# Optimization experiments

Hardware: AMD Instinct MI355X
Metric: run time of the kernel (lower is better)

The kernel has to match this reference:

```python
import jax, jax.numpy as jnp
import numpy as np

B, N, DIM, HEADS, DEPTH, MLP = 4, 1024, 256, 4, 4, 1024
DH = DIM // HEADS
EPS = 1e-5


def _ln(x, g, b):
    mu = jnp.mean(x, axis=-1, keepdims=True)
    var = jnp.mean((x - mu) ** 2, axis=-1, keepdims=True)
    return (x - mu) / jnp.sqrt(var + EPS) * g + b


def setup_inputs() -> dict:
    key = jax.random.key(0)
    ks = jax.random.split(key, 10)
    s = 0.02
    p = {}
    p["x"] = jax.random.normal(ks[0], (B, N, DIM), jnp.float32)
    p["attn_bias"] = jax.random.normal(ks[1], (2, B, HEADS, N, N), jnp.float32)
    p["ln1_g"] = jnp.ones((DEPTH, DIM), jnp.float32)
    p["ln1_b"] = jnp.zeros((DEPTH, DIM), jnp.float32)
    p["Wkv"] = jax.random.normal(ks[2], (DEPTH, DIM, 2 * DIM), jnp.float32) * s
    p["Wq"] = jax.random.normal(ks[3], (DEPTH, DIM, DIM), jnp.float32) * s
    p["Wo"] = jax.random.normal(ks[4], (DEPTH, DIM, DIM), jnp.float32) * s
    p["bo"] = jnp.zeros((DEPTH, DIM), jnp.float32)
    p["ln2_g"] = jnp.ones((DEPTH, DIM), jnp.float32)
    p["ln2_b"] = jnp.zeros((DEPTH, DIM), jnp.float32)
    p["W1"] = jax.random.normal(ks[5], (DEPTH, DIM, MLP), jnp.float32) * s
    p["b1"] = jnp.zeros((DEPTH, MLP), jnp.float32)
    p["W2"] = jax.random.normal(ks[6], (DEPTH, MLP, DIM), jnp.float32) * s
    p["b2"] = jnp.zeros((DEPTH, DIM), jnp.float32)
    p["Wg"] = jax.random.normal(ks[7], (DIM, DIM), jnp.float32) * s
    p["lng_g"] = jnp.ones((DIM,), jnp.float32)
    p["lng_b"] = jnp.zeros((DIM,), jnp.float32)
    return p


def reference(x, attn_bias, ln1_g, ln1_b, Wkv, Wq, Wo, bo, ln2_g, ln2_b, W1, b1, W2, b2, Wg, lng_g, lng_b):
    scale = DIM ** -0.5
    add_attn = attn_bias[0] + attn_bias[1]            # [B,H,N,N]
    # aggregation bias matrices are layer-invariant (recomputed identically each layer in torch)
    A = jnp.mean(attn_bias[0], axis=1)                # [B,N,N]
    S = jnp.mean(attn_bias[1], axis=1)
    G = jax.nn.softmax(A * S, axis=2)                 # [B,N,N]

    def split_heads(t):  # [B,N,DIM] -> [B,H,N,DH]
        return t.reshape(B, N, HEADS, DH).transpose(0, 2, 1, 3)

    for l in range(DEPTH):
        # softmax-GCN aggregation
        x_ma = jax.nn.relu(_ln(jnp.matmul(G, x) @ Wg, lng_g, lng_b))
        # attention (PreNorm on x only; q comes from un-normed x_ma)
        xn = _ln(x, ln1_g[l], ln1_b[l])
        kv = xn @ Wkv[l]
        k, v = jnp.split(kv, 2, axis=-1)
        q = x_ma @ Wq[l]
        qh, kh, vh = split_heads(q), split_heads(k), split_heads(v)
        dots = jnp.einsum('bhid,bhjd->bhij', qh, kh) * scale + add_attn
        attn = jax.nn.softmax(dots, axis=-1)
        out = jnp.einsum('bhij,bhjd->bhid', attn, vh)
        out = out.transpose(0, 2, 1, 3).reshape(B, N, DIM)
        x = x + out @ Wo[l] + bo[l]
        # feed-forward (exact GELU, matching torch nn.GELU default)
        xn2 = _ln(x, ln2_g[l], ln2_b[l])
        x = x + jax.nn.gelu(xn2 @ W1[l] + b1[l], approximate=False) @ W2[l] + b2[l]
    return x
```

## Files before the change

### kernel.cpp

```cpp
#include <hip/hip_runtime.h>
#include <hip/hip_bf16.h>
#include <math.h>

typedef unsigned short u16;
typedef __bf16 bf16x8 __attribute__((ext_vector_type(8)));
typedef float f32x4 __attribute__((ext_vector_type(4)));

#define B_ 4
#define N_ 1024
#define DIM_ 256
#define HEADS_ 4
#define DH_ 64
#define MLP_ 1024
#define DEPTH_ 4

__device__ __forceinline__ float r2f(u16 r){ return __uint_as_float(((unsigned)r)<<16); }
__device__ __forceinline__ u16 f2r(float f){ __hip_bfloat16 h = __float2bfloat16(f); return *(u16*)&h; }
__device__ __forceinline__ float ldv(const float* p){ return *p; }
__device__ __forceinline__ float ldv(const u16* p){ return r2f(*p); }
__device__ __forceinline__ void stv(float* p, float v){ *p = v; }
__device__ __forceinline__ void stv(u16* p, float v){ *p = f2r(v); }

__device__ __forceinline__ float gelu_exact(float v){
  return 0.5f*v*(1.0f + erff(v*0.70710678118654752440f));
}

#define MFMA16(a,b,c) __builtin_amdgcn_mfma_f32_16x16x32_bf16(a,b,c,0,0,0)

__global__ void copy_f32(const float* __restrict__ in, float* __restrict__ out, int n){
  int i = blockIdx.x*blockDim.x + threadIdx.x;
  if (i < n) out[i] = in[i];
}

__global__ void prep_bias(const float* __restrict__ bias, u16* __restrict__ G, u16* __restrict__ bsum){
  int blk = blockIdx.x;
  int i = blk & (N_-1);
  int b = blk >> 10;
  int t = threadIdx.x;
  __shared__ float sc[N_];
  __shared__ float red[256];
  long long base0 = ((long long)(b*HEADS_)*N_ + i)*(long long)N_;
  const long long hs = (long long)N_*N_;
  const long long cs = (long long)B_*HEADS_*N_*N_;
  float lmax = -3e38f;
  for (int jj=0;jj<4;jj++){
    int j = t + jj*256;
    float a = 0.f, s = 0.f;
    #pragma unroll
    for (int h=0;h<HEADS_;h++){
      float x0 = bias[base0 + h*hs + j];
      float x1 = bias[cs + base0 + h*hs + j];
      a += x0; s += x1;
      bsum[base0 + h*hs + j] = f2r(x0 + x1);
    }
    float v = (a*0.25f)*(s*0.25f);
    sc[j] = v;
    lmax = fmaxf(lmax, v);
  }
  red[t]=lmax; __syncthreads();
  for (int s=128;s>0;s>>=1){ if(t<s) red[t]=fmaxf(red[t],red[t+s]); __syncthreads(); }
  float m = red[0]; __syncthreads();
  float lsum = 0.f;
  for (int jj=0;jj<4;jj++){
    int j = t + jj*256;
    float e = __expf(sc[j]-m);
    sc[j]=e; lsum+=e;
  }
  red[t]=lsum; __syncthreads();
  for (int s=128;s>0;s>>=1){ if(t<s) red[t]+=red[t+s]; __syncthreads(); }
  float inv = 1.0f/red[0];
  u16* Grow = G + ((long long)b*N_ + i)*(long long)N_;
  for (int jj=0;jj<4;jj++){ int j=t+jj*256; Grow[j]=f2r(sc[j]*inv); }
}

template<typename TIN>
__global__ void ln_kernel(const TIN* __restrict__ X, u16* __restrict__ Y,
                          const float* __restrict__ g, const float* __restrict__ bvec, int relu){
  int row = blockIdx.x, t = threadIdx.x;
  __shared__ float red[256];
  float v = ldv(X + (long long)row*DIM_ + t);
  red[t]=v; __syncthreads();
  for (int s=128;s>0;s>>=1){ if(t<s) red[t]+=red[t+s]; __syncthreads(); }
  float mu = red[0]*(1.0f/DIM_); __syncthreads();
  float d = v - mu;
  red[t]=d*d; __syncthreads();
  for (int s=128;s>0;s>>=1){ if(t<s) red[t]+=red[t+s]; __syncthreads(); }
  float var = red[0]*(1.0f/DIM_);
  float y = d*rsqrtf(var+1e-5f)*g[t] + bvec[t];
  if (relu) y = fmaxf(y, 0.0f);
  Y[(long long)row*DIM_ + t] = f2r(y);
}

__global__ void ln_dual(const float* __restrict__ X1, const u16* __restrict__ X2,
                        u16* __restrict__ Y1, u16* __restrict__ Y2,
                        const float* __restrict__ g1, const float* __restrict__ b1v,
                        const float* __restrict__ g2, const float* __restrict__ b2v){
  int blk = blockIdx.x, t = threadIdx.x;
  bool second = blk >= B_*N_;
  int row = second ? blk - B_*N_ : blk;
  __shared__ float red[256];
  float v = second ? r2f(X2[(long long)row*DIM_ + t]) : X1[(long long)row*DIM_ + t];
  red[t]=v; __syncthreads();
  for (int s=128;s>0;s>>=1){ if(t<s) red[t]+=red[t+s]; __syncthreads(); }
  float mu = red[0]*(1.0f/DIM_); __syncthreads();
  float d = v - mu;
  red[t]=d*d; __syncthreads();
  for (int s=128;s>0;s>>=1){ if(t<s) red[t]+=red[t+s]; __syncthreads(); }
  float var = red[0]*(1.0f/DIM_);
  float y;
  if (second){ y = fmaxf(d*rsqrtf(var+1e-5f)*g2[t] + b2v[t], 0.0f); Y2[(long long)row*DIM_+t]=f2r(y); }
  else       { y = d*rsqrtf(var+1e-5f)*g1[t] + b1v[t];              Y1[(long long)row*DIM_+t]=f2r(y); }
}

template<typename TIN>
__global__ void tcast(const TIN* __restrict__ in, u16* __restrict__ out,
                      int ldin, int R, long long sIn, long long sOut){
  __shared__ float tile[32][33];
  int z = blockIdx.z;
  const TIN* I = in + (long long)z*sIn;
  u16* O = out + (long long)z*sOut;
  int c0 = blockIdx.x*32, r0 = blockIdx.y*32;
  int tx = threadIdx.x, ty = threadIdx.y;
  #pragma unroll
  for (int i=0;i<4;i++)
    tile[ty*4+i][tx] = ldv(I + (long long)(r0+ty*4+i)*ldin + c0+tx);
  __syncthreads();
  #pragma unroll
  for (int i=0;i<4;i++)
    O[(long long)(c0+ty*4+i)*R + r0+tx] = f2r(tile[tx][ty*4+i]);
}

template<typename OT, int ACT>
__global__ __launch_bounds__(256) void wgemm(
    const u16* __restrict__ A, const u16* __restrict__ BT, OT* __restrict__ Cb,
    int K, int lda, int ldbt, int ldc, int ZS,
    long long sAb, long long sAh, long long sBb, long long sBh,
    long long sCb, long long sCh,
    const float* __restrict__ colBias, const float* __restrict__ res)
{
  int z = blockIdx.z, zb = z>>ZS, zh = z & ((1<<ZS)-1);
  A  += zb*sAb + zh*sAh;
  BT += zb*sBb + zh*sBh;
  long long co = zb*sCb + zh*sCh;
  int tid = threadIdx.x, w = tid>>6, lane = tid&63;
  int lr = lane&15, qd = lane>>4;
  int m0 = blockIdx.y*64 + (w>>1)*32;
  int n0 = blockIdx.x*64 + (w&1)*32;
  const u16* Ap0 = A  + (long long)(m0+lr)*lda;
  const u16* Ap1 = A  + (long long)(m0+16+lr)*lda;
  const u16* Bp0 = BT + (long long)(n0+lr)*ldbt;
  const u16* Bp1 = BT + (long long)(n0+16+lr)*ldbt;
  f32x4 acc[2][2] = {};
  for (int k0=0; k0<K; k0+=64){
    #pragma unroll
    for (int ks=0; ks<2; ks++){
      int ko = k0 + ks*32 + qd*8;
      bf16x8 a0 = *(const bf16x8*)(Ap0+ko);
      bf16x8 a1 = *(const bf16x8*)(Ap1+ko);
      bf16x8 b0 = *(const bf16x8*)(Bp0+ko);
      bf16x8 b1 = *(const bf16x8*)(Bp1+ko);
      acc[0][0] = MFMA16(a0,b0,acc[0][0]);
      acc[0][1] = MFMA16(a0,b1,acc[0][1]);
      acc[1][0] = MFMA16(a1,b0,acc[1][0]);
      acc[1][1] = MFMA16(a1,b1,acc[1][1]);
    }
  }
  OT* C = Cb + co;
  const float* rs = res ? res + co : nullptr;
  #pragma unroll
  for (int rt=0;rt<2;rt++){
    #pragma unroll
    for (int ct=0;ct<2;ct++){
      int gc = n0 + ct*16 + lr;
      float cb = colBias ? colBias[gc] : 0.f;
      #pragma unroll
      for (int r=0;r<4;r++){
        int gr = m0 + rt*16 + qd*4 + r;
        float v = acc[rt][ct][r] + cb;
        if (ACT) v = gelu_exact(v);
        if (rs) v += rs[(long long)gr*ldc + gc];
        stv(C + (long long)gr*ldc + gc, v);
      }
    }
  }
}

static inline void gemm(hipStream_t st, const u16* A, const u16* BT, void* C, int outBf, int act,
    int M, int N, int K, int lda, int ldbt, int ldc, int Z, int ZS,
    long long sAb, long long sAh, long long sBb, long long sBh, long long sCb, long long sCh,
    const float* cb, const float* res)
{
  dim3 g(N/64, M/64, Z), b(256);
  if (outBf){
    if (act) wgemm<u16,1><<<g,b,0,st>>>(A,BT,(u16*)C,K,lda,ldbt,ldc,ZS,sAb,sAh,sBb,sBh,sCb,sCh,cb,res);
    else     wgemm<u16,0><<<g,b,0,st>>>(A,BT,(u16*)C,K,lda,ldbt,ldc,ZS,sAb,sAh,sBb,sBh,sCb,sCh,cb,res);
  } else {
    if (act) wgemm<float,1><<<g,b,0,st>>>(A,BT,(float*)C,K,lda,ldbt,ldc,ZS,sAb,sAh,sBb,sBh,sCb,sCh,cb,res);
    else     wgemm<float,0><<<g,b,0,st>>>(A,BT,(float*)C,K,lda,ldbt,ldc,ZS,sAb,sAh,sBb,sBh,sCb,sCh,cb,res);
  }
}

__global__ __launch_bounds__(256) void flash_attn(
    const u16* __restrict__ qb, const u16* __restrict__ kvb,
    const u16* __restrict__ vt, const u16* __restrict__ bsum,
    u16* __restrict__ out)
{
  int z = blockIdx.z;
  int b = z>>2, h = z&3;
  int qt = blockIdx.x;
  int tid = threadIdx.x;
  int w = tid>>6, lane = tid&63;
  int lr = lane&15, qd = lane>>4;
  __shared__ u16 Pl[4][16][72];

  int qrow0 = qt*64 + w*16;
  const u16* qp = qb + ((long long)(b*N_) + qrow0 + lr)*DIM_ + h*DH_;
  bf16x8 aq0 = *(const bf16x8*)(qp + qd*8);
  bf16x8 aq1 = *(const bf16x8*)(qp + 32 + qd*8);

  f32x4 oacc[4] = {};
  float m_r[4] = {-3e38f,-3e38f,-3e38f,-3e38f};
  float l_r[4] = {0.f,0.f,0.f,0.f};

  const u16* kbase = kvb + ((long long)(b*N_))*512 + h*DH_;
  const u16* vbase = vt + (long long)b*(DIM_*N_) + (long long)(h*DH_)*N_;
  const u16* bias_base = bsum + ((long long)z*N_ + qrow0)*(long long)N_;

  for (int jt=0; jt<16; jt++){
    int j0 = jt*64;
    f32x4 sacc[4] = {};
    #pragma unroll
    for (int nt=0; nt<4; nt++){
      const u16* kp = kbase + (long long)(j0 + nt*16 + lr)*512;
      bf16x8 bk0 = *(const bf16x8*)(kp + qd*8);
      bf16x8 bk1 = *(const bf16x8*)(kp + 32 + qd*8);
      sacc[nt] = MFMA16(aq0, bk0, sacc[nt]);
      sacc[nt] = MFMA16(aq1, bk1, sacc[nt]);
    }
    #pragma unroll
    for (int r=0;r<4;r++){
      float pv[4];
      float vmax = -3e38f;
      #pragma unroll
      for (int nt=0;nt<4;nt++){
        float v = sacc[nt][r]*0.0625f
                + r2f(bias_base[(long long)(qd*4+r)*N_ + j0 + nt*16 + lr]);
        pv[nt] = v;
        vmax = fmaxf(vmax, v);
      }
      vmax = fmaxf(vmax, __shfl_xor(vmax,1));
      vmax = fmaxf(vmax, __shfl_xor(vmax,2));
      vmax = fmaxf(vmax, __shfl_xor(vmax,4));
      vmax = fmaxf(vmax, __shfl_xor(vmax,8));
      float newm = fmaxf(m_r[r], vmax);
      float alpha = __expf(m_r[r]-newm);
      m_r[r] = newm;
      float psum = 0.f;
      #pragma unroll
      for (int nt=0;nt<4;nt++){
        float p = __expf(pv[nt]-newm);
        psum += p;
        Pl[w][qd*4+r][nt*16+lr] = f2r(p);
      }
      psum += __shfl_xor(psum,1);
      psum += __shfl_xor(psum,2);
      psum += __shfl_xor(psum,4);
      psum += __shfl_xor(psum,8);
      l_r[r] = l_r[r]*alpha + psum;
      #pragma unroll
      for (int ot=0;ot<4;ot++) oacc[ot][r] *= alpha;
    }
    #pragma unroll
    for (int ks=0;ks<2;ks++){
      bf16x8 ap = *(const bf16x8*)&Pl[w][lr][ks*32 + qd*8];
      #pragma unroll
      for (int ot=0;ot<4;ot++){
        const u16* vp = vbase + (long long)(ot*16+lr)*N_ + j0 + ks*32 + qd*8;
        bf16x8 bv = *(const bf16x8*)vp;
        oacc[ot] = MFMA16(ap, bv, oacc[ot]);
      }
    }
  }
  #pragma unroll
  for (int r=0;r<4;r++){
    float inv = 1.0f/l_r[r];
    #pragma unroll
    for (int ot=0;ot<4;ot++){
      out[((long long)(b*N_) + qrow0 + qd*4 + r)*DIM_ + h*DH_ + ot*16 + lr]
          = f2r(oacc[ot][r]*inv);
    }
  }
}

extern "C" void kernel_launch(void* const* d_in, const int* in_sizes, int n_in,
                              void* d_out, int out_size, void* d_ws, size_t ws_size,
                              hipStream_t stream){
  const float* x_in   = (const float*)d_in[0];
  const float* abias  = (const float*)d_in[1];
  const float* ln1_g  = (const float*)d_in[2];
  const float* ln1_b  = (const float*)d_in[3];
  const float* Wkv    = (const float*)d_in[4];
  const float* Wq     = (const float*)d_in[5];
  const float* Wo     = (const float*)d_in[6];
  const float* bo     = (const float*)d_in[7];
  const float* ln2_g  = (const float*)d_in[8];
  const float* ln2_b  = (const float*)d_in[9];
  const float* W1     = (const float*)d_in[10];
  const float* b1     = (const float*)d_in[11];
  const float* W2     = (const float*)d_in[12];
  const float* b2     = (const float*)d_in[13];
  const float* Wg     = (const float*)d_in[14];
  const float* lng_g  = (const float*)d_in[15];
  const float* lng_b  = (const float*)d_in[16];

  char* ws = (char*)d_ws;
  float* xf   = (float*)(ws);
  u16*  Gb    = (u16*)(ws + (4ll<<20));
  u16*  bsum  = (u16*)(ws + (12ll<<20));
  u16*  kvb   = (u16*)(ws + (44ll<<20));
  u16*  vt    = (u16*)(ws + (48ll<<20));
  u16*  xT    = (u16*)(ws + (50ll<<20));
  u16*  tmp1b = (u16*)(ws + (52ll<<20));
  u16*  tmp2b = (u16*)(ws + (54ll<<20));
  u16*  xnb   = (u16*)(ws + (56ll<<20));
  u16*  xmab  = (u16*)(ws + (58ll<<20));
  u16*  qb    = (u16*)(ws + (60ll<<20));
  u16*  aob   = (u16*)(ws + (62ll<<20));
  u16*  h1b   = (u16*)(ws + (64ll<<20));
  u16*  WkvT  = (u16*)(ws + (72ll<<20));
  u16*  WqT   = (u16*)(ws + (73ll<<20));
  u16*  WoT   = (u16*)(ws + (73ll<<20) + (512ll<<10));
  u16*  W1T   = (u16*)(ws + (74ll<<20));
  u16*  W2T   = (u16*)(ws + (76ll<<20));
  u16*  WgT   = (u16*)(ws + (78ll<<20));

  dim3 b256(256);
  dim3 tblk(32,8);
  int total = B_*N_*DIM_;

  copy_f32<<<dim3((total+255)/256), b256, 0, stream>>>(x_in, xf, total);
  prep_bias<<<dim3(B_*N_), b256, 0, stream>>>(abias, Gb, bsum);
  tcast<float><<<dim3(16,8,DEPTH_),  tblk, 0, stream>>>(Wkv, WkvT, 512, 256, 131072, 131072);
  tcast<float><<<dim3(8,8,DEPTH_),   tblk, 0, stream>>>(Wq,  WqT,  256, 256, 65536, 65536);
  tcast<float><<<dim3(8,8,DEPTH_),   tblk, 0, stream>>>(Wo,  WoT,  256, 256, 65536, 65536);
  tcast<float><<<dim3(32,8,DEPTH_),  tblk, 0, stream>>>(W1,  W1T,  1024, 256, 262144, 262144);
  tcast<float><<<dim3(8,32,DEPTH_),  tblk, 0, stream>>>(W2,  W2T,  256, 1024, 262144, 262144);
  tcast<float><<<dim3(8,8,1),        tblk, 0, stream>>>(Wg,  WgT,  256, 256, 0, 0);

  for (int l=0; l<DEPTH_; l++){
    tcast<float><<<dim3(8,32,B_), tblk, 0, stream>>>(xf, xT, 256, 1024, 262144, 262144);
    gemm(stream, Gb, xT, tmp1b, 1, 0, 1024, 256, 1024, 1024, 1024, 256, B_, 0,
         1048576,0, 262144,0, 262144,0, nullptr, nullptr);
    gemm(stream, tmp1b, WgT, tmp2b, 1, 0, 4096, 256, 256, 256, 256, 256, 1, 0,
         0,0,0,0,0,0, nullptr, nullptr);
    ln_dual<<<dim3(2*B_*N_), b256, 0, stream>>>(xf, tmp2b, xnb, xmab,
        ln1_g + l*DIM_, ln1_b + l*DIM_, lng_g, lng_b);
    gemm(stream, xnb, WkvT + (long long)l*131072, kvb, 1, 0, 4096, 512, 256, 256, 256, 512, 1, 0,
         0,0,0,0,0,0, nullptr, nullptr);
    tcast<u16><<<dim3(8,32,B_), tblk, 0, stream>>>(kvb + 256, vt, 512, 1024, 524288, 262144);
    gemm(stream, xmab, WqT + (long long)l*65536, qb, 1, 0, 4096, 256, 256, 256, 256, 256, 1, 0,
         0,0,0,0,0,0, nullptr, nullptr);
    flash_attn<<<dim3(16,1,B_*HEADS_), b256, 0, stream>>>(qb, kvb, vt, bsum, aob);
    gemm(stream, aob, WoT + (long long)l*65536, xf, 0, 0, 4096, 256, 256, 256, 256, 256, 1, 0,
         0,0,0,0,0,0, bo + l*DIM_, xf);
    ln_kernel<float><<<dim3(B_*N_), b256, 0, stream>>>(xf, xnb, ln2_g + l*DIM_, ln2_b + l*DIM_, 0);
    gemm(stream, xnb, W1T + (long long)l*262144, h1b, 1, 1, 4096, 1024, 256, 256, 256, 1024, 1, 0,
         0,0,0,0,0,0, b1 + l*MLP_, nullptr);
    float* Cdst = (l == DEPTH_-1) ? (float*)d_out : xf;
    gemm(stream, h1b, W2T + (long long)l*262144, Cdst, 0, 0, 4096, 256, 1024, 1024, 1024, 256, 1, 0,
         0,0,0,0,0,0, b2 + l*DIM_, xf);
  }
}
```

Measured before the change: 871.9 us.

## Fuse LayerNorms into full-row GEMM epilogues and merge transposes and copies

Adds a gemmln kernel in which one 64-thread wave computes a full 16x256 output row tile, so LayerNorm (and ReLU, bias, residual) runs in the GEMM epilogue. This removes the separate ln_dual and ln_kernel passes, the tmp2b buffer, the x copy and the per-layer x transpose; the W2 GEMM also writes the next layer's LN1 output and xT. The V transpose is folded into the KV GEMM epilogue, all weight transposes run in one launch, and flash attention stages its bias tile through shared memory with vector loads. In exchange, gemmln launches only 256 small single-wave blocks with 16 accumulators each, which may lower occupancy and parallelism, and its scattered transposed stores are uncoalesced.

```diff
diff --git a/kernel.cpp b/kernel.cpp
--- a/kernel.cpp
+++ b/kernel.cpp
@@ -16,8 +16,6 @@
 
 __device__ __forceinline__ float r2f(u16 r){ return __uint_as_float(((unsigned)r)<<16); }
 __device__ __forceinline__ u16 f2r(float f){ __hip_bfloat16 h = __float2bfloat16(f); return *(u16*)&h; }
-__device__ __forceinline__ float ldv(const float* p){ return *p; }
-__device__ __forceinline__ float ldv(const u16* p){ return r2f(*p); }
 __device__ __forceinline__ void stv(float* p, float v){ *p = v; }
 __device__ __forceinline__ void stv(u16* p, float v){ *p = f2r(v); }
 
@@ -26,11 +24,6 @@
 }
 
 #define MFMA16(a,b,c) __builtin_amdgcn_mfma_f32_16x16x32_bf16(a,b,c,0,0,0)
-
-__global__ void copy_f32(const float* __restrict__ in, float* __restrict__ out, int n){
-  int i = blockIdx.x*blockDim.x + threadIdx.x;
-  if (i < n) out[i] = in[i];
-}
 
 __global__ void prep_bias(const float* __restrict__ bias, u16* __restrict__ G, u16* __restrict__ bsum){
   int blk = blockIdx.x;
@@ -73,12 +66,11 @@
   for (int jj=0;jj<4;jj++){ int j=t+jj*256; Grow[j]=f2r(sc[j]*inv); }
 }
 
-template<typename TIN>
-__global__ void ln_kernel(const TIN* __restrict__ X, u16* __restrict__ Y,
-                          const float* __restrict__ g, const float* __restrict__ bvec, int relu){
+__global__ void ln_kernel(const float* __restrict__ X, u16* __restrict__ Y,
+                          const float* __restrict__ g, const float* __restrict__ bvec){
   int row = blockIdx.x, t = threadIdx.x;
   __shared__ float red[256];
-  float v = ldv(X + (long long)row*DIM_ + t);
+  float v = X[(long long)row*DIM_ + t];
   red[t]=v; __syncthreads();
   for (int s=128;s>0;s>>=1){ if(t<s) red[t]+=red[t+s]; __syncthreads(); }
   float mu = red[0]*(1.0f/DIM_); __syncthreads();
@@ -86,44 +78,30 @@
   red[t]=d*d; __syncthreads();
   for (int s=128;s>0;s>>=1){ if(t<s) red[t]+=red[t+s]; __syncthreads(); }
   float var = red[0]*(1.0f/DIM_);
-  float y = d*rsqrtf(var+1e-5f)*g[t] + bvec[t];
-  if (relu) y = fmaxf(y, 0.0f);
-  Y[(long long)row*DIM_ + t] = f2r(y);
-}
-
-__global__ void ln_dual(const float* __restrict__ X1, const u16* __restrict__ X2,
-                        u16* __restrict__ Y1, u16* __restrict__ Y2,
-                        const float* __restrict__ g1, const float* __restrict__ b1v,
-                        const float* __restrict__ g2, const float* __restrict__ b2v){
-  int blk = blockIdx.x, t = threadIdx.x;
-  bool second = blk >= B_*N_;
-  int row = second ? blk - B_*N_ : blk;
-  __shared__ float red[256];
-  float v = second ? r2f(X2[(long long)row*DIM_ + t]) : X1[(long long)row*DIM_ + t];
-  red[t]=v; __syncthreads();
-  for (int s=128;s>0;s>>=1){ if(t<s) red[t]+=red[t+s]; __syncthreads(); }
-  float mu = red[0]*(1.0f/DIM_); __syncthreads();
-  float d = v - mu;
-  red[t]=d*d; __syncthreads();
-  for (int s=128;s>0;s>>=1){ if(t<s) red[t]+=red[t+s]; __syncthreads(); }
-  float var = red[0]*(1.0f/DIM_);
-  float y;
-  if (second){ y = fmaxf(d*rsqrtf(var+1e-5f)*g2[t] + b2v[t], 0.0f); Y2[(long long)row*DIM_+t]=f2r(y); }
-  else       { y = d*rsqrtf(var+1e-5f)*g1[t] + b1v[t];              Y1[(long long)row*DIM_+t]=f2r(y); }
-}
-
-template<typename TIN>
-__global__ void tcast(const TIN* __restrict__ in, u16* __restrict__ out,
-                      int ldin, int R, long long sIn, long long sOut){
+  Y[(long long)row*DIM_ + t] = f2r(d*rsqrtf(var+1e-5f)*g[t] + bvec[t]);
+}
+
+__global__ void tcast_all(const float* __restrict__ Wkv, const float* __restrict__ Wq,
+                          const float* __restrict__ Wo, const float* __restrict__ W1,
+                          const float* __restrict__ W2, const float* __restrict__ Wg,
+                          const float* __restrict__ xin,
+                          u16* WkvT, u16* WqT, u16* WoT, u16* W1T, u16* W2T, u16* WgT, u16* xT){
+  int z = blockIdx.z;
+  const float* I; u16* O; int ldin, R, C;
+  if (z < 4)       { I = Wkv + z*131072;      O = WkvT + z*131072;      ldin=512;  R=256;  C=512;  }
+  else if (z < 8)  { I = Wq  + (z-4)*65536;   O = WqT  + (z-4)*65536;   ldin=256;  R=256;  C=256;  }
+  else if (z < 12) { I = Wo  + (z-8)*65536;   O = WoT  + (z-8)*65536;   ldin=256;  R=256;  C=256;  }
+  else if (z < 16) { I = W1  + (z-12)*262144; O = W1T  + (z-12)*262144; ldin=1024; R=256;  C=1024; }
+  else if (z < 20) { I = W2  + (z-16)*262144; O = W2T  + (z-16)*262144; ldin=256;  R=1024; C=256;  }
+  else if (z == 20){ I = Wg;                  O = WgT;                  ldin=256;  R=256;  C=256;  }
+  else             { I = xin + (z-21)*262144; O = xT   + (z-21)*262144; ldin=256;  R=1024; C=256;  }
+  int c0 = blockIdx.x*32, r0 = blockIdx.y*32;
+  if (c0 >= C || r0 >= R) return;
   __shared__ float tile[32][33];
-  int z = blockIdx.z;
-  const TIN* I = in + (long long)z*sIn;
-  u16* O = out + (long long)z*sOut;
-  int c0 = blockIdx.x*32, r0 = blockIdx.y*32;
   int tx = threadIdx.x, ty = threadIdx.y;
   #pragma unroll
   for (int i=0;i<4;i++)
-    tile[ty*4+i][tx] = ldv(I + (long long)(r0+ty*4+i)*ldin + c0+tx);
+    tile[ty*4+i][tx] = I[(long long)(r0+ty*4+i)*ldin + c0+tx];
   __syncthreads();
   #pragma unroll
   for (int i=0;i<4;i++)
@@ -136,7 +114,8 @@
     int K, int lda, int ldbt, int ldc, int ZS,
     long long sAb, long long sAh, long long sBb, long long sBh,
     long long sCb, long long sCh,
-    const float* __restrict__ colBias, const float* __restrict__ res)
+    const float* __restrict__ colBias, const float* __restrict__ res,
+    u16* __restrict__ vt)
 {
   int z = blockIdx.z, zb = z>>ZS, zh = z & ((1<<ZS)-1);
   A  += zb*sAb + zh*sAh;
@@ -180,6 +159,10 @@
         if (ACT) v = gelu_exact(v);
         if (rs) v += rs[(long long)gr*ldc + gc];
         stv(C + (long long)gr*ldc + gc, v);
+        if (vt && gc >= 256){
+          int b = gr>>10, rl = gr&1023;
+          vt[(long long)b*262144 + (long long)(gc-256)*1024 + rl] = f2r(v);
+        }
       }
     }
   }
@@ -188,15 +171,78 @@
 static inline void gemm(hipStream_t st, const u16* A, const u16* BT, void* C, int outBf, int act,
     int M, int N, int K, int lda, int ldbt, int ldc, int Z, int ZS,
     long long sAb, long long sAh, long long sBb, long long sBh, long long sCb, long long sCh,
-    const float* cb, const float* res)
+    const float* cb, const float* res, u16* vt)
 {
   dim3 g(N/64, M/64, Z), b(256);
   if (outBf){
-    if (act) wgemm<u16,1><<<g,b,0,st>>>(A,BT,(u16*)C,K,lda,ldbt,ldc,ZS,sAb,sAh,sBb,sBh,sCb,sCh,cb,res);
-    else     wgemm<u16,0><<<g,b,0,st>>>(A,BT,(u16*)C,K,lda,ldbt,ldc,ZS,sAb,sAh,sBb,sBh,sCb,sCh,cb,res);
+    if (act) wgemm<u16,1><<<g,b,0,st>>>(A,BT,(u16*)C,K,lda,ldbt,ldc,ZS,sAb,sAh,sBb,sBh,sCb,sCh,cb,res,vt);
+    else     wgemm<u16,0><<<g,b,0,st>>>(A,BT,(u16*)C,K,lda,ldbt,ldc,ZS,sAb,sAh,sBb,sBh,sCb,sCh,cb,res,vt);
   } else {
-    if (act) wgemm<float,1><<<g,b,0,st>>>(A,BT,(float*)C,K,lda,ldbt,ldc,ZS,sAb,sAh,sBb,sBh,sCb,sCh,cb,res);
-    else     wgemm<float,0><<<g,b,0,st>>>(A,BT,(float*)C,K,lda,ldbt,ldc,ZS,sAb,sAh,sBb,sBh,sCb,sCh,cb,res);
+    if (act) wgemm<float,1><<<g,b,0,st>>>(A,BT,(float*)C,K,lda,ldbt,ldc,ZS,sAb,sAh,sBb,sBh,sCb,sCh,cb,res,vt);
+    else     wgemm<float,0><<<g,b,0,st>>>(A,BT,(float*)C,K,lda,ldbt,ldc,ZS,sAb,sAh,sBb,sBh,sCb,sCh,cb,res,vt);
+  }
+}
+
+template<int MODE>
+__global__ __launch_bounds__(64) void gemmln(
+    const u16* __restrict__ A, const u16* __restrict__ BT, int K, int ldbt,
+    const float* __restrict__ colBias, const float* __restrict__ res,
+    float* __restrict__ fout,
+    const float* __restrict__ lng, const float* __restrict__ lnb,
+    u16* __restrict__ lnOut, u16* __restrict__ xTout)
+{
+  int lane = threadIdx.x;
+  int lr = lane&15, qd = lane>>4;
+  int m0 = blockIdx.x*16;
+  const u16* Ap = A + (long long)(m0+lr)*K;
+  f32x4 acc[16] = {};
+  for (int k0=0;k0<K;k0+=32){
+    bf16x8 af = *(const bf16x8*)(Ap + k0 + qd*8);
+    #pragma unroll
+    for (int ct=0;ct<16;ct++){
+      bf16x8 bfv = *(const bf16x8*)(BT + (long long)(ct*16+lr)*ldbt + k0 + qd*8);
+      acc[ct] = MFMA16(af, bfv, acc[ct]);
+    }
+  }
+  #pragma unroll
+  for (int r=0;r<4;r++){
+    int row = m0 + qd*4 + r;
+    float v[16];
+    #pragma unroll
+    for (int ct=0;ct<16;ct++){
+      float x = acc[ct][r];
+      if (MODE>=1){ int col = ct*16+lr; x += colBias[col] + res[(long long)row*DIM_ + col]; }
+      v[ct] = x;
+    }
+    if (MODE>=1){
+      #pragma unroll
+      for (int ct=0;ct<16;ct++) fout[(long long)row*DIM_ + ct*16+lr] = v[ct];
+    }
+    if (MODE==2 && xTout){
+      int b = row>>10, rl = row&1023;
+      #pragma unroll
+      for (int ct=0;ct<16;ct++)
+        xTout[(long long)b*262144 + (long long)(ct*16+lr)*1024 + rl] = f2r(v[ct]);
+    }
+    if (MODE==0 || lnOut){
+      float s=0.f;
+      #pragma unroll
+      for (int ct=0;ct<16;ct++) s += v[ct];
+      s += __shfl_xor(s,1); s += __shfl_xor(s,2); s += __shfl_xor(s,4); s += __shfl_xor(s,8);
+      float mu = s*(1.0f/256.0f);
+      float s2=0.f;
+      #pragma unroll
+      for (int ct=0;ct<16;ct++){ float d=v[ct]-mu; s2 += d*d; }
+      s2 += __shfl_xor(s2,1); s2 += __shfl_xor(s2,2); s2 += __shfl_xor(s2,4); s2 += __shfl_xor(s2,8);
+      float rstd = rsqrtf(s2*(1.0f/256.0f)+1e-5f);
+      #pragma unroll
+      for (int ct=0;ct<16;ct++){
+        int col = ct*16+lr;
+        float y = (v[ct]-mu)*rstd*lng[col] + lnb[col];
+        if (MODE==0) y = fmaxf(y,0.f);
+        lnOut[(long long)row*DIM_ + col] = f2r(y);
+      }
+    }
   }
 }
 
@@ -212,6 +258,7 @@
   int w = tid>>6, lane = tid&63;
   int lr = lane&15, qd = lane>>4;
   __shared__ u16 Pl[4][16][72];
+  __shared__ u16 sb[4][16][72];
 
   int qrow0 = qt*64 + w*16;
   const u16* qp = qb + ((long long)(b*N_) + qrow0 + lr)*DIM_ + h*DH_;
@@ -225,9 +272,17 @@
   const u16* kbase = kvb + ((long long)(b*N_))*512 + h*DH_;
   const u16* vbase = vt + (long long)b*(DIM_*N_) + (long long)(h*DH_)*N_;
   const u16* bias_base = bsum + ((long long)z*N_ + qrow0)*(long long)N_;
+  int srr = lane>>2, scc = (lane&3)*16;
 
   for (int jt=0; jt<16; jt++){
     int j0 = jt*64;
+    {
+      const u16* gs = bias_base + (long long)srr*N_ + j0 + scc;
+      uint4 t0 = *(const uint4*)gs;
+      uint4 t1 = *(const uint4*)(gs+8);
+      *(uint4*)&sb[w][srr][scc]   = t0;
+      *(uint4*)&sb[w][srr][scc+8] = t1;
+    }
     f32x4 sacc[4] = {};
     #pragma unroll
     for (int nt=0; nt<4; nt++){
@@ -243,8 +298,7 @@
       float vmax = -3e38f;
       #pragma unroll
       for (int nt=0;nt<4;nt++){
-        float v = sacc[nt][r]*0.0625f
-                + r2f(bias_base[(long long)(qd*4+r)*N_ + j0 + nt*16 + lr]);
+        float v = sacc[nt][r]*0.0625f + r2f(sb[w][qd*4+r][nt*16+lr]);
         pv[nt] = v;
         vmax = fmaxf(vmax, v);
       }
@@ -321,53 +375,46 @@
   u16*  vt    = (u16*)(ws + (48ll<<20));
   u16*  xT    = (u16*)(ws + (50ll<<20));
   u16*  tmp1b = (u16*)(ws + (52ll<<20));
-  u16*  tmp2b = (u16*)(ws + (54ll<<20));
-  u16*  xnb   = (u16*)(ws + (56ll<<20));
-  u16*  xmab  = (u16*)(ws + (58ll<<20));
-  u16*  qb    = (u16*)(ws + (60ll<<20));
-  u16*  aob   = (u16*)(ws + (62ll<<20));
-  u16*  h1b   = (u16*)(ws + (64ll<<20));
-  u16*  WkvT  = (u16*)(ws + (72ll<<20));
-  u16*  WqT   = (u16*)(ws + (73ll<<20));
-  u16*  WoT   = (u16*)(ws + (73ll<<20) + (512ll<<10));
-  u16*  W1T   = (u16*)(ws + (74ll<<20));
-  u16*  W2T   = (u16*)(ws + (76ll<<20));
-  u16*  WgT   = (u16*)(ws + (78ll<<20));
+  u16*  xnb   = (u16*)(ws + (54ll<<20));
+  u16*  xmab  = (u16*)(ws + (56ll<<20));
+  u16*  qb    = (u16*)(ws + (58ll<<20));
+  u16*  aob   = (u16*)(ws + (60ll<<20));
+  u16*  h1b   = (u16*)(ws + (62ll<<20));
+  u16*  WkvT  = (u16*)(ws + (70ll<<20));
+  u16*  WqT   = (u16*)(ws + (71ll<<20));
+  u16*  WoT   = (u16*)(ws + (71ll<<20) + (512ll<<10));
+  u16*  W1T   = (u16*)(ws + (72ll<<20));
+  u16*  W2T   = (u16*)(ws + (74ll<<20));
+  u16*  WgT   = (u16*)(ws + (76ll<<20));
 
   dim3 b256(256);
-  dim3 tblk(32,8);
-  int total = B_*N_*DIM_;
-
-  copy_f32<<<dim3((total+255)/256), b256, 0, stream>>>(x_in, xf, total);
+
   prep_bias<<<dim3(B_*N_), b256, 0, stream>>>(abias, Gb, bsum);
-  tcast<float><<<dim3(16,8,DEPTH_),  tblk, 0, stream>>>(Wkv, WkvT, 512, 256, 131072, 131072);
-  tcast<float><<<dim3(8,8,DEPTH_),   tblk, 0, stream>>>(Wq,  WqT,  256, 256, 65536, 65536);
-  tcast<float><<<dim3(8,8,DEPTH_),   tblk, 0, stream>>>(Wo,  WoT,  256, 256, 65536, 65536);
-  tcast<float><<<dim3(32,8,DEPTH_),  tblk, 0, stream>>>(W1,  W1T,  1024, 256, 262144, 262144);
-  tcast<float><<<dim3(8,32,DEPTH_),  tblk, 0, stream>>>(W2,  W2T,  256, 1024, 262144, 262144);
-  tcast<float><<<dim3(8,8,1),        tblk, 0, stream>>>(Wg,  WgT,  256, 256, 0, 0);
+  tcast_all<<<dim3(32,32,25), dim3(32,8), 0, stream>>>(Wkv,Wq,Wo,W1,W2,Wg,x_in,
+                                                       WkvT,WqT,WoT,W1T,W2T,WgT,xT);
+  ln_kernel<<<dim3(B_*N_), b256, 0, stream>>>(x_in, xnb, ln1_g, ln1_b);
 
   for (int l=0; l<DEPTH_; l++){
-    tcast<float><<<dim3(8,32,B_), tblk, 0, stream>>>(xf, xT, 256, 1024, 262144, 262144);
+    const float* resx = (l==0) ? x_in : xf;
     gemm(stream, Gb, xT, tmp1b, 1, 0, 1024, 256, 1024, 1024, 1024, 256, B_, 0,
-         1048576,0, 262144,0, 262144,0, nullptr, nullptr);
-    gemm(stream, tmp1b, WgT, tmp2b, 1, 0, 4096, 256, 256, 256, 256, 256, 1, 0,
-         0,0,0,0,0,0, nullptr, nullptr);
-    ln_dual<<<dim3(2*B_*N_), b256, 0, stream>>>(xf, tmp2b, xnb, xmab,
-        ln1_g + l*DIM_, ln1_b + l*DIM_, lng_g, lng_b);
+         1048576,0, 262144,0, 262144,0, nullptr, nullptr, nullptr);
+    gemmln<0><<<dim3(256), dim3(64), 0, stream>>>(tmp1b, WgT, 256, 256,
+        nullptr, nullptr, nullptr, lng_g, lng_b, xmab, nullptr);
     gemm(stream, xnb, WkvT + (long long)l*131072, kvb, 1, 0, 4096, 512, 256, 256, 256, 512, 1, 0,
-         0,0,0,0,0,0, nullptr, nullptr);
-    tcast<u16><<<dim3(8,32,B_), tblk, 0, stream>>>(kvb + 256, vt, 512, 1024, 524288, 262144);
+         0,0,0,0,0,0, nullptr, nullptr, vt);
     gemm(stream, xmab, WqT + (long long)l*65536, qb, 1, 0, 4096, 256, 256, 256, 256, 256, 1, 0,
-         0,0,0,0,0,0, nullptr, nullptr);
+         0,0,0,0,0,0, nullptr, nullptr, nullptr);
     flash_attn<<<dim3(16,1,B_*HEADS_), b256, 0, stream>>>(qb, kvb, vt, bsum, aob);
-    gemm(stream, aob, WoT + (long long)l*65536, xf, 0, 0, 4096, 256, 256, 256, 256, 256, 1, 0,
-         0,0,0,0,0,0, bo + l*DIM_, xf);
-    ln_kernel<float><<<dim3(B_*N_), b256, 0, stream>>>(xf, xnb, ln2_g + l*DIM_, ln2_b + l*DIM_, 0);
+    gemmln<1><<<dim3(256), dim3(64), 0, stream>>>(aob, WoT + (long long)l*65536, 256, 256,
+        bo + l*DIM_, resx, xf, ln2_g + l*DIM_, ln2_b + l*DIM_, xnb, nullptr);
     gemm(stream, xnb, W1T + (long long)l*262144, h1b, 1, 1, 4096, 1024, 256, 256, 256, 1024, 1, 0,
-         0,0,0,0,0,0, b1 + l*MLP_, nullptr);
-    float* Cdst = (l == DEPTH_-1) ? (float*)d_out : xf;
-    gemm(stream, h1b, W2T + (long long)l*262144, Cdst, 0, 0, 4096, 256, 1024, 1024, 1024, 256, 1, 0,
-         0,0,0,0,0,0, b2 + l*DIM_, xf);
-  }
-}
+         0,0,0,0,0,0, b1 + l*MLP_, nullptr, nullptr);
+    if (l < DEPTH_-1){
+      gemmln<2><<<dim3(256), dim3(64), 0, stream>>>(h1b, W2T + (long long)l*262144, 1024, 1024,
+          b2 + l*DIM_, xf, xf, ln1_g + (l+1)*DIM_, ln1_b + (l+1)*DIM_, xnb, xT);
+    } else {
+      gemmln<2><<<dim3(256), dim3(64), 0, stream>>>(h1b, W2T + (long long)l*262144, 1024, 1024,
+          b2 + l*DIM_, xf, (float*)d_out, nullptr, nullptr, nullptr, nullptr);
+    }
+  }
+}
```

After: 846.6 us. 2.9% less time.
